# Kernel tuning notes

Hardware: AMD Instinct MI355X
Metric: run time of the kernel (lower is better)

The kernel has to match this reference:

```python
import jax, jax.numpy as jnp
import numpy as np

B, N = 16384, 1024

def setup_inputs() -> dict:
    key = jax.random.key(0)
    k1, k2, k3, k4 = jax.random.split(key, 4)
    mu1 = jax.random.normal(k1, (B, N), dtype=jnp.float32)
    mu2 = jax.random.normal(k2, (B, N), dtype=jnp.float32)
    # variances must be positive; floor at 0.1
    var_1 = jax.random.uniform(k3, (B, N), dtype=jnp.float32) + 0.1
    var_2 = jax.random.uniform(k4, (B, N), dtype=jnp.float32) + 0.1
    return {"mu1": mu1, "mu2": mu2, "var_1": var_1, "var_2": var_2}

def reference(mu1, mu2, var_1, var_2):
    # KL( N(mu1, diag(var_1)) || N(mu2, diag(var_2)) ), exploiting diagonal structure.
    # term_1 = log(det(S2)/det(S1)) = sum(log var_2) - sum(log var_1)
    term_1 = jnp.sum(jnp.log(var_2) - jnp.log(var_1), axis=-1)
    # term_2 = trace(S2^{-1} S1) = sum(var_1 / var_2)
    term_2 = jnp.sum(var_1 / var_2, axis=-1)
    # term_3 = (mu2-mu1)^T S2^{-1} (mu2-mu1)
    diff = mu2 - mu1
    term_3 = jnp.sum(diff * diff / var_2, axis=-1)
    n = mu1.shape[1]
    kl = 0.5 * (term_1 - n + term_2 + term_3)  # [B]
    return jnp.mean(kl)  # reduction='mean'
```

## Files before the change

### kernel.cpp

```cpp
#include <hip/hip_runtime.h>

#define BLOCKS  2048
#define THREADS 256
#define WAVES   (THREADS / 64)

__global__ __launch_bounds__(THREADS) void kl_partial_kernel(
    const float4* __restrict__ mu1, const float4* __restrict__ mu2,
    const float4* __restrict__ v1,  const float4* __restrict__ v2,
    float* __restrict__ partial, int n4)
{
    float acc = 0.0f;
    const int stride = gridDim.x * blockDim.x;
    for (int i = blockIdx.x * blockDim.x + threadIdx.x; i < n4; i += stride) {
        float4 a  = mu1[i];
        float4 b  = mu2[i];
        float4 s1 = v1[i];
        float4 s2 = v2[i];

        {
            float r = __builtin_amdgcn_rcpf(s2.x);
            float d = b.x - a.x;
            acc += __logf(s2.x) - __logf(s1.x) + s1.x * r + d * d * r;
        }
        {
            float r = __builtin_amdgcn_rcpf(s2.y);
            float d = b.y - a.y;
            acc += __logf(s2.y) - __logf(s1.y) + s1.y * r + d * d * r;
        }
        {
            float r = __builtin_amdgcn_rcpf(s2.z);
            float d = b.z - a.z;
            acc += __logf(s2.z) - __logf(s1.z) + s1.z * r + d * d * r;
        }
        {
            float r = __builtin_amdgcn_rcpf(s2.w);
            float d = b.w - a.w;
            acc += __logf(s2.w) - __logf(s1.w) + s1.w * r + d * d * r;
        }
    }

    #pragma unroll
    for (int off = 32; off > 0; off >>= 1)
        acc += __shfl_down(acc, off, 64);

    __shared__ float sm[WAVES];
    const int lane = threadIdx.x & 63;
    const int wave = threadIdx.x >> 6;
    if (lane == 0) sm[wave] = acc;
    __syncthreads();
    if (threadIdx.x == 0) {
        float s = 0.0f;
        #pragma unroll
        for (int w = 0; w < WAVES; ++w) s += sm[w];
        partial[blockIdx.x] = s;
    }
}

__global__ __launch_bounds__(THREADS) void kl_final_kernel(
    const float* __restrict__ partial, float* __restrict__ out,
    int nblocks, float invB, float nDim)
{
    double acc = 0.0;
    for (int i = threadIdx.x; i < nblocks; i += THREADS)
        acc += (double)partial[i];

    #pragma unroll
    for (int off = 32; off > 0; off >>= 1)
        acc += __shfl_down(acc, off, 64);

    __shared__ double sm[WAVES];
    const int lane = threadIdx.x & 63;
    const int wave = threadIdx.x >> 6;
    if (lane == 0) sm[wave] = acc;
    __syncthreads();
    if (threadIdx.x == 0) {
        double s = 0.0;
        #pragma unroll
        for (int w = 0; w < WAVES; ++w) s += sm[w];
        out[0] = (float)(0.5 * (s * (double)invB - (double)nDim));
    }
}

extern "C" void kernel_launch(void* const* d_in, const int* in_sizes, int n_in,
                              void* d_out, int out_size, void* d_ws, size_t ws_size,
                              hipStream_t stream)
{
    const float4* mu1 = (const float4*)d_in[0];
    const float4* mu2 = (const float4*)d_in[1];
    const float4* v1  = (const float4*)d_in[2];
    const float4* v2  = (const float4*)d_in[3];

    const long long total = (long long)in_sizes[0];
    const int n4 = (int)(total / 4);
    const int B = 16384;
    const int N = 1024;

    float* partial = (float*)d_ws;
    float* out = (float*)d_out;

    kl_partial_kernel<<<BLOCKS, THREADS, 0, stream>>>(mu1, mu2, v1, v2, partial, n4);
    kl_final_kernel<<<1, THREADS, 0, stream>>>(partial, out, BLOCKS,
                                               1.0f / (float)B, (float)N);
}
```

Before: 241.2 us.

## Batch per-thread loads across fixed tiles and fuse the two logs into one

Replaces the grid-stride loop with a fixed grid in which each thread issues four float4 loads per input array up front, raising the number of memory requests in flight. It also rewrites log(v2)-log(v1)+v1/v2 as t-log(t) with t=v1/v2, halving the transcendental count, and splits accumulation into two independent chains. The indexing assumes the element count equals BLOCKS*THREADS*ITER*4 and has no bounds check, so other shapes would break.

```diff
diff --git a/kernel.cpp b/kernel.cpp
--- a/kernel.cpp
+++ b/kernel.cpp
@@ -1,7 +1,8 @@
 #include <hip/hip_runtime.h>
 
-#define BLOCKS  2048
 #define THREADS 256
+#define ITER    4
+#define BLOCKS  4096
 #define WAVES   (THREADS / 64)
 
 __global__ __launch_bounds__(THREADS) void kl_partial_kernel(
@@ -9,35 +10,58 @@
     const float4* __restrict__ v1,  const float4* __restrict__ v2,
     float* __restrict__ partial, int n4)
 {
-    float acc = 0.0f;
-    const int stride = gridDim.x * blockDim.x;
-    for (int i = blockIdx.x * blockDim.x + threadIdx.x; i < n4; i += stride) {
-        float4 a  = mu1[i];
-        float4 b  = mu2[i];
-        float4 s1 = v1[i];
-        float4 s2 = v2[i];
+    const int base = blockIdx.x * (THREADS * ITER) + threadIdx.x;
 
+    float4 a[ITER], b[ITER], x1[ITER], x2[ITER];
+
+    #pragma unroll
+    for (int j = 0; j < ITER; ++j) {
+        const int i = base + j * THREADS;
+        x2[j] = v2[i];
+    }
+    #pragma unroll
+    for (int j = 0; j < ITER; ++j) {
+        const int i = base + j * THREADS;
+        x1[j] = v1[i];
+    }
+    #pragma unroll
+    for (int j = 0; j < ITER; ++j) {
+        const int i = base + j * THREADS;
+        a[j] = mu1[i];
+        b[j] = mu2[i];
+    }
+
+    float acc0 = 0.0f, acc1 = 0.0f;
+
+    #pragma unroll
+    for (int j = 0; j < ITER; ++j) {
         {
-            float r = __builtin_amdgcn_rcpf(s2.x);
-            float d = b.x - a.x;
-            acc += __logf(s2.x) - __logf(s1.x) + s1.x * r + d * d * r;
+            float r = __builtin_amdgcn_rcpf(x2[j].x);
+            float t = x1[j].x * r;
+            float d = b[j].x - a[j].x;
+            acc0 += (t - __logf(t)) + d * d * r;
         }
         {
-            float r = __builtin_amdgcn_rcpf(s2.y);
-            float d = b.y - a.y;
-            acc += __logf(s2.y) - __logf(s1.y) + s1.y * r + d * d * r;
+            float r = __builtin_amdgcn_rcpf(x2[j].y);
+            float t = x1[j].y * r;
+            float d = b[j].y - a[j].y;
+            acc1 += (t - __logf(t)) + d * d * r;
         }
         {
-            float r = __builtin_amdgcn_rcpf(s2.z);
-            float d = b.z - a.z;
-            acc += __logf(s2.z) - __logf(s1.z) + s1.z * r + d * d * r;
+            float r = __builtin_amdgcn_rcpf(x2[j].z);
+            float t = x1[j].z * r;
+            float d = b[j].z - a[j].z;
+            acc0 += (t - __logf(t)) + d * d * r;
         }
         {
-            float r = __builtin_amdgcn_rcpf(s2.w);
-            float d = b.w - a.w;
-            acc += __logf(s2.w) - __logf(s1.w) + s1.w * r + d * d * r;
+            float r = __builtin_amdgcn_rcpf(x2[j].w);
+            float t = x1[j].w * r;
+            float d = b[j].w - a[j].w;
+            acc1 += (t - __logf(t)) + d * d * r;
         }
     }
+
+    float acc = acc0 + acc1;
 
     #pragma unroll
     for (int off = 32; off > 0; off >>= 1)
```

Result: no change. 241.4 us (+0.1%).

## Unroll fixed per-block tiles with nontemporal loads and single-log KL term

Applied to the files above, without the earlier changes.

Replaces the grid-stride loop with a fixed 4-iteration unrolled tile per thread over 4096 blocks. All four loads in each iteration are issued up front as nontemporal loads. The two logs per element are merged into one by computing t = var1/var2 and using t - log(t), and the work is split across two accumulators. The goal is more memory-level parallelism, less cache pollution and fewer transcendental ops. The cost is that the bounds check is gone, so the grid must exactly cover the input size.

```diff
diff --git a/kernel.cpp b/kernel.cpp
--- a/kernel.cpp
+++ b/kernel.cpp
@@ -1,43 +1,56 @@
 #include <hip/hip_runtime.h>
 
-#define BLOCKS  2048
 #define THREADS 256
+#define ITER    4
+#define BLOCKS  4096
 #define WAVES   (THREADS / 64)
 
+typedef float f4 __attribute__((ext_vector_type(4)));
+
 __global__ __launch_bounds__(THREADS) void kl_partial_kernel(
-    const float4* __restrict__ mu1, const float4* __restrict__ mu2,
-    const float4* __restrict__ v1,  const float4* __restrict__ v2,
+    const f4* __restrict__ mu1, const f4* __restrict__ mu2,
+    const f4* __restrict__ v1,  const f4* __restrict__ v2,
     float* __restrict__ partial, int n4)
 {
-    float acc = 0.0f;
-    const int stride = gridDim.x * blockDim.x;
-    for (int i = blockIdx.x * blockDim.x + threadIdx.x; i < n4; i += stride) {
-        float4 a  = mu1[i];
-        float4 b  = mu2[i];
-        float4 s1 = v1[i];
-        float4 s2 = v2[i];
+    const int base = blockIdx.x * (THREADS * ITER) + threadIdx.x;
+
+    float acc0 = 0.0f, acc1 = 0.0f;
+
+    #pragma unroll
+    for (int j = 0; j < ITER; ++j) {
+        const int i = base + j * THREADS;
+        f4 s2 = __builtin_nontemporal_load(&v2[i]);
+        f4 s1 = __builtin_nontemporal_load(&v1[i]);
+        f4 a  = __builtin_nontemporal_load(&mu1[i]);
+        f4 b  = __builtin_nontemporal_load(&mu2[i]);
 
         {
             float r = __builtin_amdgcn_rcpf(s2.x);
+            float t = s1.x * r;
             float d = b.x - a.x;
-            acc += __logf(s2.x) - __logf(s1.x) + s1.x * r + d * d * r;
+            acc0 += (t - __logf(t)) + d * d * r;
         }
         {
             float r = __builtin_amdgcn_rcpf(s2.y);
+            float t = s1.y * r;
             float d = b.y - a.y;
-            acc += __logf(s2.y) - __logf(s1.y) + s1.y * r + d * d * r;
+            acc1 += (t - __logf(t)) + d * d * r;
         }
         {
             float r = __builtin_amdgcn_rcpf(s2.z);
+            float t = s1.z * r;
             float d = b.z - a.z;
-            acc += __logf(s2.z) - __logf(s1.z) + s1.z * r + d * d * r;
+            acc0 += (t - __logf(t)) + d * d * r;
         }
         {
             float r = __builtin_amdgcn_rcpf(s2.w);
+            float t = s1.w * r;
             float d = b.w - a.w;
-            acc += __logf(s2.w) - __logf(s1.w) + s1.w * r + d * d * r;
+            acc1 += (t - __logf(t)) + d * d * r;
         }
     }
+
+    float acc = acc0 + acc1;
 
     #pragma unroll
     for (int off = 32; off > 0; off >>= 1)
@@ -85,10 +98,10 @@
                               void* d_out, int out_size, void* d_ws, size_t ws_size,
                               hipStream_t stream)
 {
-    const float4* mu1 = (const float4*)d_in[0];
-    const float4* mu2 = (const float4*)d_in[1];
-    const float4* v1  = (const float4*)d_in[2];
-    const float4* v2  = (const float4*)d_in[3];
+    const f4* mu1 = (const f4*)d_in[0];
+    const f4* mu2 = (const f4*)d_in[1];
+    const f4* v1  = (const f4*)d_in[2];
+    const f4* v2  = (const f4*)d_in[3];
 
     const long long total = (long long)in_sizes[0];
     const int n4 = (int)(total / 4);
```

Result: faster. 214.2 us (-11.2%).
